# Performance work log

Hardware: AMD Instinct MI355X
Metric: run time of the kernel (lower is better)

Reference implementation:

```python
import jax, jax.numpy as jnp
import numpy as np

B_SZ, N_NODES, C_IN, C_OUT, M_EDGES, DEG = 32, 4096, 64, 64, 64, 256
E_INC = M_EDGES * DEG  # 16384 incidences
NEG_SLOPE = 0.2
MARGIN = 4.2


def setup_inputs() -> dict:
    key = jax.random.key(0)
    k1, k2, k3, k4 = jax.random.split(key, 4)
    x = jax.random.normal(k1, (B_SZ, N_NODES, C_IN), jnp.float32)
    # glorot-ish params
    weight = jax.random.normal(k2, (C_IN, C_OUT), jnp.float32) * (1.0 / np.sqrt(C_IN))
    att = jax.random.normal(k3, (1, 1, 2 * C_OUT), jnp.float32) * 0.1
    node_ids = jax.random.randint(k4, (E_INC,), 0, N_NODES, dtype=jnp.int32)
    edge_ids = jnp.repeat(jnp.arange(M_EDGES, dtype=jnp.int32), DEG)  # sorted, all edges present
    hyperedge_index = jnp.stack([node_ids, edge_ids], axis=0)
    return {"x": x, "weight": weight, "att": att,
            "hyperedge_index": hyperedge_index,
            "num_edges": M_EDGES, "num_nodes": N_NODES}


def _segment_softmax(scores, seg, num_segments):
    m = jax.ops.segment_max(scores, seg, num_segments=num_segments)
    e = jnp.exp(scores - m[seg])
    s = jax.ops.segment_sum(e, seg, num_segments=num_segments)
    return e / s[seg]


def reference(x, weight, att, hyperedge_index, num_edges, num_nodes):
    node_ids = hyperedge_index[0]
    edge_ids = hyperedge_index[1]
    M = num_edges
    N = num_nodes

    xw = jnp.einsum('bnc,cd->bnd', x, weight)       # [B,N,C]
    x1 = jnp.swapaxes(xw, 0, 1)                     # [N,B,C]

    x_i = x1[node_ids]                              # [E,B,C] gather per incidence
    edge_sums = jax.ops.segment_sum(x_i, edge_ids, num_segments=M,
                                    indices_are_sorted=True)  # [M,B,C]
    x_j = edge_sums[edge_ids]                       # [E,B,C]

    # pairwise hyperedge contrastive loss (vectorized double loop over edges)
    inner = jnp.einsum('kbc,mbc->kmb', edge_sums, edge_sums)          # [M,M,B]
    nrm = jnp.linalg.norm(edge_sums, axis=-1)                         # [M,B]
    cos = inner / (nrm[:, None, :] * nrm[None, :, :])                 # [M,M,B]
    diff = edge_sums[:, None] - edge_sums[None, :]                    # [M,M,B,C]
    dist = jnp.linalg.norm(diff, axis=-1)                             # [M,M,B]
    loss_item = cos * dist + (1.0 - cos) * jnp.clip(MARGIN - dist, 0.0)
    loss_hyper = jnp.sum(jnp.abs(jnp.mean(loss_item, axis=2))) / (M + 1) ** 2

    # GAT-style attention over incidences, softmax grouped by node
    cat = jnp.concatenate([x_i, x_j], axis=-1)                        # [E,B,2C]
    scores = jnp.sum(cat * att[0], axis=-1)                           # [E,B] (heads=1)
    scores = jax.nn.leaky_relu(scores, negative_slope=NEG_SLOPE)
    alpha = _segment_softmax(scores, node_ids, N)                     # [E,B]
    # dropout omitted (eval mode)

    ones = jnp.ones((node_ids.shape[0],), xw.dtype)
    D = jax.ops.segment_sum(ones, node_ids, num_segments=N)           # node degree
    deg_e = jax.ops.segment_sum(ones, edge_ids, num_segments=M, indices_are_sorted=True)
    B_norm = jnp.where(deg_e > 0, 1.0 / deg_e, 0.0)                   # 1/edge degree, inf->0

    # stage 1: nodes -> hyperedges (source_to_target)
    msg1 = B_norm[edge_ids][:, None, None] * (alpha[..., None] * x_i) # [E,B,C]
    out_e = jax.ops.segment_sum(msg1, edge_ids, num_segments=M, indices_are_sorted=True)
    # stage 2: hyperedges -> nodes (target_to_source)
    msg2 = D[node_ids][:, None, None] * (alpha[..., None] * out_e[edge_ids])
    out_n = jax.ops.segment_sum(msg2, node_ids, num_segments=N)       # [N,B,C]

    out = jnp.swapaxes(out_n, 0, 1)                                   # [B,N,C]
    constrain_total = jnp.abs(jnp.mean(x_i - x_j)) + loss_hyper
    return out, constrain_total
```

## Files before the change

kernel.cpp:

```cpp
#include <hip/hip_runtime.h>
#include <math.h>

#define B_SZ 32
#define N_NODES 4096
#define C_DIM 64
#define M_EDGES 64
#define DEG 256
#define E_INC 16384
#define NEG_SLOPE 0.2f
#define MARGIN 4.2f

__device__ __forceinline__ float wsum64(float v) {
#pragma unroll
  for (int off = 32; off > 0; off >>= 1) v += __shfl_xor(v, off, 64);
  return v;
}

__device__ __forceinline__ float4 redq16_32(float4 a) {
#pragma unroll
  for (int off = 16; off < 64; off <<= 1) {
    a.x += __shfl_xor(a.x, off, 64);
    a.y += __shfl_xor(a.y, off, 64);
    a.z += __shfl_xor(a.z, off, 64);
    a.w += __shfl_xor(a.w, off, 64);
  }
  return a;
}

union SmemBig {
  struct {
    float wl[4096];
    float sx[4][64];
    float sxc[64];
  } e;
  struct {
    int cnt[N_NODES];
  } c;
  struct {
    float part[4][64];
    float wattl[64];
  } s;
};

__global__ __launch_bounds__(256) void k_p1(
    const float* __restrict__ x, const float* __restrict__ w,
    const float* __restrict__ att, const int* __restrict__ node_ids,
    float* __restrict__ s1_t, float* __restrict__ es_t,
    float* __restrict__ s2, float* __restrict__ nrm2,
    float* __restrict__ essum, int* __restrict__ cntv) {
  __shared__ SmemBig sm;
  const int bid = blockIdx.x;
  const int t = threadIdx.x;
  if (bid < 2048) {
    const int b = 4 * (bid & 7) + ((bid >> 3) & 3);
    const int m = bid >> 5;
    const int lane = t & 63, wv = t >> 6;
    const int qc = lane & 15, rsub = lane >> 4;
    float4* wl4 = (float4*)sm.e.wl;
    const float4* w4 = (const float4*)w;
#pragma unroll
    for (int i = 0; i < 4; ++i) wl4[t + 256 * i] = w4[t + 256 * i];
    const float4* xb4 = (const float4*)(x + (size_t)b * (N_NODES * C_DIM));
    const int rbase = m * DEG + wv * 64 + rsub;
    float4 acc = {0.f, 0.f, 0.f, 0.f};
#pragma unroll
    for (int i = 0; i < 16; ++i) {
      const int node = node_ids[rbase + i * 4];
      const float4 xv = xb4[node * 16 + qc];
      acc.x += xv.x;
      acc.y += xv.y;
      acc.z += xv.z;
      acc.w += xv.w;
    }
    acc = redq16_32(acc);
    if (rsub == 0) ((float4*)sm.e.sx[wv])[qc] = acc;
    __syncthreads();
    if (t < 64) {
      sm.e.sxc[t] =
          sm.e.sx[0][t] + sm.e.sx[1][t] + sm.e.sx[2][t] + sm.e.sx[3][t];
      float es = 0.f;
#pragma unroll 8
      for (int j = 0; j < 64; ++j)
        es = fmaf(sm.e.sxc[j], sm.e.wl[j * 64 + t], es);
      es_t[(m * 64 + t) * 32 + b] = es;
      const float sr = wsum64(es * att[64 + t]);
      const float nr = wsum64(es * es);
      const float er = wsum64(es);
      if (t == 0) {
        s2[m * 32 + b] = sr;
        nrm2[m * 32 + b] = nr;
        essum[m * 32 + b] = er;
      }
    }
  } else if (bid < 2112) {
    const int m = bid - 2048;
#pragma unroll
    for (int i = 0; i < 16; ++i) sm.c.cnt[t + 256 * i] = 0;
    __syncthreads();
    atomicAdd(&sm.c.cnt[node_ids[m * DEG + t]], 1);
    __syncthreads();
#pragma unroll
    for (int i = 0; i < 16; ++i)
      cntv[m * N_NODES + t + 256 * i] = sm.c.cnt[t + 256 * i];
  } else {
    const int sb = bid - 2112;
    const int kk = t & 63, q = t >> 6;
    float p = 0.f;
#pragma unroll
    for (int c = 0; c < 16; ++c)
      p = fmaf(w[kk * 64 + q * 16 + c], att[q * 16 + c], p);
    sm.s.part[q][kk] = p;
    __syncthreads();
    if (t < 64)
      sm.s.wattl[t] =
          sm.s.part[0][t] + sm.s.part[1][t] + sm.s.part[2][t] + sm.s.part[3][t];
    __syncthreads();
    const int lane = t & 63, wv = t >> 6;
    const int kq = lane & 15, rsub = lane >> 4;
    const float4 wq = ((const float4*)sm.s.wattl)[kq];
    const int r0 = sb * 256 + wv * 64;
#pragma unroll 4
    for (int it = 0; it < 16; ++it) {
      const int row = r0 + it * 4 + rsub;
      const float4 xv = ((const float4*)x)[row * 16 + kq];
      float vv = xv.x * wq.x + xv.y * wq.y + xv.z * wq.z + xv.w * wq.w;
      vv += __shfl_xor(vv, 1, 64);
      vv += __shfl_xor(vv, 2, 64);
      vv += __shfl_xor(vv, 4, 64);
      vv += __shfl_xor(vv, 8, 64);
      if (kq == 0) {
        const int n = row & (N_NODES - 1);
        const int b = row >> 12;
        s1_t[n * 32 + b] = vv;
      }
    }
  }
}

__global__ __launch_bounds__(256) void k_p2(
    const float* __restrict__ es_t, const float* __restrict__ nrm2,
    const int* __restrict__ cntv, const float* __restrict__ s1_t,
    const float* __restrict__ s2, float* __restrict__ lossbuf,
    float2* __restrict__ pnb) {
  const int bid = blockIdx.x;
  if (bid < 1024) {
    const int wv = threadIdx.x >> 6;
    const int p = bid * 4 + wv;
    const int k = p >> 6, m = p & 63;
    const int lane = threadIdx.x & 63;
    const int b = lane & 31, ch = lane >> 5;
    float inner = 0.f;
#pragma unroll 8
    for (int cc = 0; cc < 32; ++cc) {
      const int c = cc + 32 * ch;
      inner = fmaf(es_t[(k * 64 + c) * 32 + b], es_t[(m * 64 + c) * 32 + b],
                   inner);
    }
    inner += __shfl_xor(inner, 32, 64);
    const float nk2 = nrm2[k * 32 + b];
    const float nm2 = nrm2[m * 32 + b];
    const float d2 = fmaxf(nk2 + nm2 - 2.f * inner, 0.f);
    const float dist = sqrtf(d2);
    const float cosv = inner / sqrtf(nk2 * nm2);
    float li = cosv * dist + (1.f - cosv) * fmaxf(MARGIN - dist, 0.f);
#pragma unroll
    for (int off = 16; off > 0; off >>= 1) li += __shfl_xor(li, off, 64);
    if (lane == 0) lossbuf[p] = fabsf(li * (1.f / 32.f));
  } else {
    const int idx = (bid - 1024) * 256 + threadIdx.x;
    const int n = idx >> 5, b = idx & 31;
    const float s1v = s1_t[n * 32 + b];
    float mx = -1e30f, S = 0.f;
#pragma unroll 4
    for (int m = 0; m < 64; ++m) {
      const int cm = cntv[m * N_NODES + n];
      if (cm > 0) {
        float sc = s1v + s2[m * 32 + b];
        sc = sc > 0.f ? sc : NEG_SLOPE * sc;
        const float nm = fmaxf(mx, sc);
        S = S * __expf(mx - nm) + (float)cm * __expf(sc - nm);
        mx = nm;
      }
    }
    float2 pv;
    pv.x = mx;
    pv.y = (S > 0.f) ? 1.f / S : 0.f;
    pnb[n * 32 + b] = pv;
  }
}

__global__ __launch_bounds__(256) void k_p3(
    const float* __restrict__ x, const int* __restrict__ node_ids,
    const float* __restrict__ w, const float* __restrict__ s1_t,
    const float* __restrict__ s2, const float2* __restrict__ pnb,
    const float* __restrict__ essum, const float* __restrict__ lossbuf,
    float* __restrict__ out_e_t, float* __restrict__ outs) {
  __shared__ SmemBig sm;
  const int bid = blockIdx.x;
  const int t = threadIdx.x;
  if (bid < 2048) {
    const int b = 4 * (bid & 7) + ((bid >> 3) & 3);
    const int m = bid >> 5;
    const int lane = t & 63, wv = t >> 6;
    const int qc = lane & 15, rsub = lane >> 4;
    float4* wl4 = (float4*)sm.e.wl;
    const float4* w4 = (const float4*)w;
#pragma unroll
    for (int i = 0; i < 4; ++i) wl4[t + 256 * i] = w4[t + 256 * i];
    const float4* xb4 = (const float4*)(x + (size_t)b * (N_NODES * C_DIM));
    const float s2mb = s2[m * 32 + b];
    const int rbase = m * DEG + wv * 64 + rsub;
    float4 acc = {0.f, 0.f, 0.f, 0.f};
#pragma unroll
    for (int i = 0; i < 16; ++i) {
      const int node = node_ids[rbase + i * 4];
      const float s1v = s1_t[node * 32 + b];
      const float2 pv = pnb[node * 32 + b];
      float sc = s1v + s2mb;
      sc = sc > 0.f ? sc : NEG_SLOPE * sc;
      const float a = __expf(sc - pv.x) * pv.y;
      const float4 xv = xb4[node * 16 + qc];
      acc.x = fmaf(a, xv.x, acc.x);
      acc.y = fmaf(a, xv.y, acc.y);
      acc.z = fmaf(a, xv.z, acc.z);
      acc.w = fmaf(a, xv.w, acc.w);
    }
    acc = redq16_32(acc);
    if (rsub == 0) ((float4*)sm.e.sx[wv])[qc] = acc;
    __syncthreads();
    if (t < 64) {
      sm.e.sxc[t] =
          sm.e.sx[0][t] + sm.e.sx[1][t] + sm.e.sx[2][t] + sm.e.sx[3][t];
      float oc = 0.f;
#pragma unroll 8
      for (int j = 0; j < 64; ++j)
        oc = fmaf(sm.e.sxc[j], sm.e.wl[j * 64 + t], oc);
      out_e_t[(m * 64 + t) * 32 + b] = oc * (1.0f / 256.0f);
    }
  } else {
    __shared__ float smf[256];
    float s = 0.f;
    for (int i = t; i < M_EDGES * B_SZ; i += 256) s += essum[i];
    smf[t] = s;
    __syncthreads();
    for (int o = 128; o > 0; o >>= 1) {
      if (t < o) smf[t] += smf[t + o];
      __syncthreads();
    }
    const float S = smf[0];
    __syncthreads();
    float l = 0.f;
    for (int i = t; i < M_EDGES * M_EDGES; i += 256) l += lossbuf[i];
    smf[t] = l;
    __syncthreads();
    for (int o = 128; o > 0; o >>= 1) {
      if (t < o) smf[t] += smf[t + o];
      __syncthreads();
    }
    if (t == 0) {
      const float mean = S * (-255.0f) / 33554432.0f;
      outs[0] = fabsf(mean) + smf[0] * (1.0f / 4225.0f);
    }
  }
}

__global__ __launch_bounds__(256) void k_p4(
    const int* __restrict__ cntv, const float* __restrict__ s1_t,
    const float* __restrict__ s2, const float2* __restrict__ pnb,
    const float* __restrict__ out_e_t, float* __restrict__ out) {
  __shared__ int listm[64];
  __shared__ int cl[64];
  __shared__ float al[64][32];
  __shared__ float DnS;
  __shared__ int llenS;
  const int n = blockIdx.x;
  const int t = threadIdx.x;
  if (t < 64) {
    const int cv = cntv[t * N_NODES + n];
    cl[t] = cv;
    const unsigned long long mask = __ballot(cv > 0);
    const int pos = __popcll(mask & ((1ull << t) - 1ull));
    if (cv > 0) listm[pos] = t;
    const float d = wsum64((float)cv);
    if (t == 0) {
      llenS = __popcll(mask);
      DnS = d;
    }
  }
  __syncthreads();
  const int llen = llenS;
  const int c = t & 63, bq = t >> 6;
  const size_t nb = (size_t)n * 64 + c;
  const size_t st = (size_t)N_NODES * 64;
  if (llen == 0) {
#pragma unroll
    for (int j = 0; j < 8; ++j) out[(bq * 8 + j) * st + nb] = 0.f;
    return;
  }
  {
    const int b = t & 31, lq = t >> 5;
    const float s1v = s1_t[n * 32 + b];
    const float2 pv = pnb[n * 32 + b];
    for (int base = 0; base < llen; base += 8) {
      const int li = base + lq;
      if (li < llen) {
        const int m = listm[li];
        float sc = s1v + s2[m * 32 + b];
        sc = sc > 0.f ? sc : NEG_SLOPE * sc;
        al[li][b] = (float)cl[m] * __expf(sc - pv.x) * pv.y;
      }
    }
  }
  __syncthreads();
  float4 a0 = {0.f, 0.f, 0.f, 0.f}, a1 = {0.f, 0.f, 0.f, 0.f};
  for (int li = 0; li < llen; ++li) {
    const int m = listm[li];
    const float4 v0 = *(const float4*)&out_e_t[(m * 64 + c) * 32 + bq * 8];
    const float4 v1 = *(const float4*)&out_e_t[(m * 64 + c) * 32 + bq * 8 + 4];
    const float* alr = al[li];
    a0.x = fmaf(alr[bq * 8 + 0], v0.x, a0.x);
    a0.y = fmaf(alr[bq * 8 + 1], v0.y, a0.y);
    a0.z = fmaf(alr[bq * 8 + 2], v0.z, a0.z);
    a0.w = fmaf(alr[bq * 8 + 3], v0.w, a0.w);
    a1.x = fmaf(alr[bq * 8 + 4], v1.x, a1.x);
    a1.y = fmaf(alr[bq * 8 + 5], v1.y, a1.y);
    a1.z = fmaf(alr[bq * 8 + 6], v1.z, a1.z);
    a1.w = fmaf(alr[bq * 8 + 7], v1.w, a1.w);
  }
  const float Dn = DnS;
  out[(bq * 8 + 0) * st + nb] = Dn * a0.x;
  out[(bq * 8 + 1) * st + nb] = Dn * a0.y;
  out[(bq * 8 + 2) * st + nb] = Dn * a0.z;
  out[(bq * 8 + 3) * st + nb] = Dn * a0.w;
  out[(bq * 8 + 4) * st + nb] = Dn * a1.x;
  out[(bq * 8 + 5) * st + nb] = Dn * a1.y;
  out[(bq * 8 + 6) * st + nb] = Dn * a1.z;
  out[(bq * 8 + 7) * st + nb] = Dn * a1.w;
}

extern "C" void kernel_launch(void* const* d_in, const int* in_sizes, int n_in,
                              void* d_out, int out_size, void* d_ws,
                              size_t ws_size, hipStream_t stream) {
  (void)in_sizes; (void)n_in; (void)out_size; (void)ws_size;
  const float* x = (const float*)d_in[0];
  const float* weight = (const float*)d_in[1];
  const float* att = (const float*)d_in[2];
  const int* node_ids = (const int*)d_in[3];
  float* out = (float*)d_out;

  char* wsb = (char*)d_ws;
  float* es_t = (float*)(wsb);
  float* out_e_t = (float*)(wsb + (512 << 10));
  float* s1_t = (float*)(wsb + (1024 << 10));
  int* cntv = (int*)(wsb + (1536 << 10));
  float2* pnb = (float2*)(wsb + (2560 << 10));
  float* s2 = (float*)(wsb + (3584 << 10));
  float* nrm2 = (float*)(wsb + (3592 << 10));
  float* essum = (float*)(wsb + (3600 << 10));
  float* lossbuf = (float*)(wsb + (3608 << 10));

  k_p1<<<2624, 256, 0, stream>>>(x, weight, att, node_ids, s1_t, es_t, s2,
                                 nrm2, essum, cntv);
  k_p2<<<1536, 256, 0, stream>>>(es_t, nrm2, cntv, s1_t, s2, lossbuf, pnb);
  k_p3<<<2049, 256, 0, stream>>>(x, node_ids, weight, s1_t, s2, pnb, essum,
                                 lossbuf, out_e_t,
                                 out + (size_t)B_SZ * N_NODES * C_DIM);
  k_p4<<<4096, 256, 0, stream>>>(cntv, s1_t, s2, pnb, out_e_t, out);
}
```

Baseline: 91.44 us.

## Fuse attention score into gather, exploit loss symmetry, precompute node edge lists

New measurement: 102.7 us. +12.3%, slower.

```diff
diff --git a/kernel.cpp b/kernel.cpp
--- a/kernel.cpp
+++ b/kernel.cpp
@@ -27,19 +27,9 @@
   return a;
 }
 
-union SmemBig {
-  struct {
-    float wl[4096];
-    float sx[4][64];
-    float sxc[64];
-  } e;
-  struct {
-    int cnt[N_NODES];
-  } c;
-  struct {
-    float part[4][64];
-    float wattl[64];
-  } s;
+union U16K {
+  float wl[4096];
+  int cnt[4096];
 };
 
 __global__ __launch_bounds__(256) void k_p1(
@@ -48,7 +38,11 @@
     float* __restrict__ s1_t, float* __restrict__ es_t,
     float* __restrict__ s2, float* __restrict__ nrm2,
     float* __restrict__ essum, int* __restrict__ cntv) {
-  __shared__ SmemBig sm;
+  __shared__ U16K u;
+  __shared__ float part[4][64];
+  __shared__ float wattl[64];
+  __shared__ float sx[4][64];
+  __shared__ float sxc[64];
   const int bid = blockIdx.x;
   const int t = threadIdx.x;
   if (bid < 2048) {
@@ -56,10 +50,23 @@
     const int m = bid >> 5;
     const int lane = t & 63, wv = t >> 6;
     const int qc = lane & 15, rsub = lane >> 4;
-    float4* wl4 = (float4*)sm.e.wl;
+    float4* wl4 = (float4*)u.wl;
     const float4* w4 = (const float4*)w;
 #pragma unroll
     for (int i = 0; i < 4; ++i) wl4[t + 256 * i] = w4[t + 256 * i];
+    {
+      const int kk = t & 63, q = t >> 6;
+      float p = 0.f;
+#pragma unroll
+      for (int c = 0; c < 16; ++c)
+        p = fmaf(w[kk * 64 + q * 16 + c], att[q * 16 + c], p);
+      part[q][kk] = p;
+    }
+    __syncthreads();
+    if (t < 64)
+      wattl[t] = part[0][t] + part[1][t] + part[2][t] + part[3][t];
+    __syncthreads();
+    const float4 wq = ((const float4*)wattl)[qc];
     const float4* xb4 = (const float4*)(x + (size_t)b * (N_NODES * C_DIM));
     const int rbase = m * DEG + wv * 64 + rsub;
     float4 acc = {0.f, 0.f, 0.f, 0.f};
@@ -71,17 +78,21 @@
       acc.y += xv.y;
       acc.z += xv.z;
       acc.w += xv.w;
+      float sv = xv.x * wq.x + xv.y * wq.y + xv.z * wq.z + xv.w * wq.w;
+      sv += __shfl_xor(sv, 1, 64);
+      sv += __shfl_xor(sv, 2, 64);
+      sv += __shfl_xor(sv, 4, 64);
+      sv += __shfl_xor(sv, 8, 64);
+      if (qc == 0) s1_t[node * 32 + b] = sv;
     }
     acc = redq16_32(acc);
-    if (rsub == 0) ((float4*)sm.e.sx[wv])[qc] = acc;
+    if (rsub == 0) ((float4*)sx[wv])[qc] = acc;
     __syncthreads();
     if (t < 64) {
-      sm.e.sxc[t] =
-          sm.e.sx[0][t] + sm.e.sx[1][t] + sm.e.sx[2][t] + sm.e.sx[3][t];
+      sxc[t] = sx[0][t] + sx[1][t] + sx[2][t] + sx[3][t];
       float es = 0.f;
 #pragma unroll 8
-      for (int j = 0; j < 64; ++j)
-        es = fmaf(sm.e.sxc[j], sm.e.wl[j * 64 + t], es);
+      for (int j = 0; j < 64; ++j) es = fmaf(sxc[j], u.wl[j * 64 + t], es);
       es_t[(m * 64 + t) * 32 + b] = es;
       const float sr = wsum64(es * att[64 + t]);
       const float nr = wsum64(es * es);
@@ -92,61 +103,35 @@
         essum[m * 32 + b] = er;
       }
     }
-  } else if (bid < 2112) {
+  } else {
     const int m = bid - 2048;
 #pragma unroll
-    for (int i = 0; i < 16; ++i) sm.c.cnt[t + 256 * i] = 0;
-    __syncthreads();
-    atomicAdd(&sm.c.cnt[node_ids[m * DEG + t]], 1);
+    for (int i = 0; i < 16; ++i) u.cnt[t + 256 * i] = 0;
+    __syncthreads();
+    atomicAdd(&u.cnt[node_ids[m * DEG + t]], 1);
     __syncthreads();
 #pragma unroll
     for (int i = 0; i < 16; ++i)
-      cntv[m * N_NODES + t + 256 * i] = sm.c.cnt[t + 256 * i];
-  } else {
-    const int sb = bid - 2112;
-    const int kk = t & 63, q = t >> 6;
-    float p = 0.f;
-#pragma unroll
-    for (int c = 0; c < 16; ++c)
-      p = fmaf(w[kk * 64 + q * 16 + c], att[q * 16 + c], p);
-    sm.s.part[q][kk] = p;
-    __syncthreads();
-    if (t < 64)
-      sm.s.wattl[t] =
-          sm.s.part[0][t] + sm.s.part[1][t] + sm.s.part[2][t] + sm.s.part[3][t];
-    __syncthreads();
-    const int lane = t & 63, wv = t >> 6;
-    const int kq = lane & 15, rsub = lane >> 4;
-    const float4 wq = ((const float4*)sm.s.wattl)[kq];
-    const int r0 = sb * 256 + wv * 64;
-#pragma unroll 4
-    for (int it = 0; it < 16; ++it) {
-      const int row = r0 + it * 4 + rsub;
-      const float4 xv = ((const float4*)x)[row * 16 + kq];
-      float vv = xv.x * wq.x + xv.y * wq.y + xv.z * wq.z + xv.w * wq.w;
-      vv += __shfl_xor(vv, 1, 64);
-      vv += __shfl_xor(vv, 2, 64);
-      vv += __shfl_xor(vv, 4, 64);
-      vv += __shfl_xor(vv, 8, 64);
-      if (kq == 0) {
-        const int n = row & (N_NODES - 1);
-        const int b = row >> 12;
-        s1_t[n * 32 + b] = vv;
-      }
-    }
+      cntv[m * N_NODES + t + 256 * i] = u.cnt[t + 256 * i];
   }
 }
 
 __global__ __launch_bounds__(256) void k_p2(
     const float* __restrict__ es_t, const float* __restrict__ nrm2,
     const int* __restrict__ cntv, const float* __restrict__ s1_t,
-    const float* __restrict__ s2, float* __restrict__ lossbuf,
-    float2* __restrict__ pnb) {
+    const float* __restrict__ s2, float* __restrict__ lossbuf2,
+    float2* __restrict__ pnb, int* __restrict__ pdat,
+    int* __restrict__ plen) {
   const int bid = blockIdx.x;
-  if (bid < 1024) {
+  if (bid < 504) {
     const int wv = threadIdx.x >> 6;
     const int p = bid * 4 + wv;
-    const int k = p >> 6, m = p & 63;
+    int k = 0, off = 0;
+    while (off + (63 - k) <= p) {
+      off += 63 - k;
+      ++k;
+    }
+    const int m = k + 1 + (p - off);
     const int lane = threadIdx.x & 63;
     const int b = lane & 31, ch = lane >> 5;
     float inner = 0.f;
@@ -164,24 +149,33 @@
     const float cosv = inner / sqrtf(nk2 * nm2);
     float li = cosv * dist + (1.f - cosv) * fmaxf(MARGIN - dist, 0.f);
 #pragma unroll
-    for (int off = 16; off > 0; off >>= 1) li += __shfl_xor(li, off, 64);
-    if (lane == 0) lossbuf[p] = fabsf(li * (1.f / 32.f));
+    for (int o = 16; o > 0; o >>= 1) li += __shfl_xor(li, o, 64);
+    if (lane == 0) lossbuf2[p] = 2.f * fabsf(li * (1.f / 32.f));
   } else {
-    const int idx = (bid - 1024) * 256 + threadIdx.x;
+    const int idx = (bid - 504) * 256 + threadIdx.x;
     const int n = idx >> 5, b = idx & 31;
     const float s1v = s1_t[n * 32 + b];
+    const bool leader = (b == 0);
     float mx = -1e30f, S = 0.f;
+    int j = 0, Dsum = 0;
 #pragma unroll 4
     for (int m = 0; m < 64; ++m) {
       const int cm = cntv[m * N_NODES + n];
-      if (cm > 0) {
-        float sc = s1v + s2[m * 32 + b];
-        sc = sc > 0.f ? sc : NEG_SLOPE * sc;
-        const float nm = fmaxf(mx, sc);
-        S = S * __expf(mx - nm) + (float)cm * __expf(sc - nm);
-        mx = nm;
+      float sc = s1v + s2[m * 32 + b];
+      sc = sc > 0.f ? sc : NEG_SLOPE * sc;
+      const float scv = (cm > 0) ? sc : -1e30f;
+      const float nm = fmaxf(mx, scv);
+      S = S * __expf(mx - nm) + (float)cm * __expf(scv - nm);
+      mx = nm;
+      if (leader) {
+        if (cm > 0) {
+          pdat[n * 64 + j] = m | (cm << 8);
+          ++j;
+        }
+        Dsum += cm;
       }
     }
+    if (leader) plen[n] = j | (Dsum << 7);
     float2 pv;
     pv.x = mx;
     pv.y = (S > 0.f) ? 1.f / S : 0.f;
@@ -193,9 +187,11 @@
     const float* __restrict__ x, const int* __restrict__ node_ids,
     const float* __restrict__ w, const float* __restrict__ s1_t,
     const float* __restrict__ s2, const float2* __restrict__ pnb,
-    const float* __restrict__ essum, const float* __restrict__ lossbuf,
+    const float* __restrict__ essum, const float* __restrict__ lossbuf2,
     float* __restrict__ out_e_t, float* __restrict__ outs) {
-  __shared__ SmemBig sm;
+  __shared__ U16K u;
+  __shared__ float sx[4][64];
+  __shared__ float sxc[64];
   const int bid = blockIdx.x;
   const int t = threadIdx.x;
   if (bid < 2048) {
@@ -203,7 +199,7 @@
     const int m = bid >> 5;
     const int lane = t & 63, wv = t >> 6;
     const int qc = lane & 15, rsub = lane >> 4;
-    float4* wl4 = (float4*)sm.e.wl;
+    float4* wl4 = (float4*)u.wl;
     const float4* w4 = (const float4*)w;
 #pragma unroll
     for (int i = 0; i < 4; ++i) wl4[t + 256 * i] = w4[t + 256 * i];
@@ -226,15 +222,13 @@
       acc.w = fmaf(a, xv.w, acc.w);
     }
     acc = redq16_32(acc);
-    if (rsub == 0) ((float4*)sm.e.sx[wv])[qc] = acc;
+    if (rsub == 0) ((float4*)sx[wv])[qc] = acc;
     __syncthreads();
     if (t < 64) {
-      sm.e.sxc[t] =
-          sm.e.sx[0][t] + sm.e.sx[1][t] + sm.e.sx[2][t] + sm.e.sx[3][t];
+      sxc[t] = sx[0][t] + sx[1][t] + sx[2][t] + sx[3][t];
       float oc = 0.f;
 #pragma unroll 8
-      for (int j = 0; j < 64; ++j)
-        oc = fmaf(sm.e.sxc[j], sm.e.wl[j * 64 + t], oc);
+      for (int j = 0; j < 64; ++j) oc = fmaf(sxc[j], u.wl[j * 64 + t], oc);
       out_e_t[(m * 64 + t) * 32 + b] = oc * (1.0f / 256.0f);
     }
   } else {
@@ -250,7 +244,7 @@
     const float S = smf[0];
     __syncthreads();
     float l = 0.f;
-    for (int i = t; i < M_EDGES * M_EDGES; i += 256) l += lossbuf[i];
+    for (int i = t; i < 2016; i += 256) l += lossbuf2[i];
     smf[t] = l;
     __syncthreads();
     for (int o = 128; o > 0; o >>= 1) {
@@ -265,56 +259,50 @@
 }
 
 __global__ __launch_bounds__(256) void k_p4(
-    const int* __restrict__ cntv, const float* __restrict__ s1_t,
-    const float* __restrict__ s2, const float2* __restrict__ pnb,
-    const float* __restrict__ out_e_t, float* __restrict__ out) {
-  __shared__ int listm[64];
-  __shared__ int cl[64];
+    const int* __restrict__ plen, const int* __restrict__ pdat,
+    const float* __restrict__ s1_t, const float* __restrict__ s2,
+    const float2* __restrict__ pnb, const float* __restrict__ out_e_t,
+    float* __restrict__ out) {
+  __shared__ int lme[64];
+  __shared__ float lcnt[64];
   __shared__ float al[64][32];
-  __shared__ float DnS;
-  __shared__ int llenS;
   const int n = blockIdx.x;
   const int t = threadIdx.x;
-  if (t < 64) {
-    const int cv = cntv[t * N_NODES + n];
-    cl[t] = cv;
-    const unsigned long long mask = __ballot(cv > 0);
-    const int pos = __popcll(mask & ((1ull << t) - 1ull));
-    if (cv > 0) listm[pos] = t;
-    const float d = wsum64((float)cv);
-    if (t == 0) {
-      llenS = __popcll(mask);
-      DnS = d;
-    }
-  }
-  __syncthreads();
-  const int llen = llenS;
+  const int pl = plen[n];
+  const int len = pl & 127;
+  const float Dn = (float)(pl >> 7);
   const int c = t & 63, bq = t >> 6;
   const size_t nb = (size_t)n * 64 + c;
   const size_t st = (size_t)N_NODES * 64;
-  if (llen == 0) {
+  if (len == 0) {
 #pragma unroll
     for (int j = 0; j < 8; ++j) out[(bq * 8 + j) * st + nb] = 0.f;
     return;
   }
+  if (t < len) {
+    const int pe = pdat[n * 64 + t];
+    lme[t] = pe & 63;
+    lcnt[t] = (float)(pe >> 8);
+  }
+  __syncthreads();
   {
     const int b = t & 31, lq = t >> 5;
     const float s1v = s1_t[n * 32 + b];
     const float2 pv = pnb[n * 32 + b];
-    for (int base = 0; base < llen; base += 8) {
+    for (int base = 0; base < len; base += 8) {
       const int li = base + lq;
-      if (li < llen) {
-        const int m = listm[li];
+      if (li < len) {
+        const int m = lme[li];
         float sc = s1v + s2[m * 32 + b];
         sc = sc > 0.f ? sc : NEG_SLOPE * sc;
-        al[li][b] = (float)cl[m] * __expf(sc - pv.x) * pv.y;
+        al[li][b] = lcnt[li] * __expf(sc - pv.x) * pv.y;
       }
     }
   }
   __syncthreads();
   float4 a0 = {0.f, 0.f, 0.f, 0.f}, a1 = {0.f, 0.f, 0.f, 0.f};
-  for (int li = 0; li < llen; ++li) {
-    const int m = listm[li];
+  for (int li = 0; li < len; ++li) {
+    const int m = lme[li];
     const float4 v0 = *(const float4*)&out_e_t[(m * 64 + c) * 32 + bq * 8];
     const float4 v1 = *(const float4*)&out_e_t[(m * 64 + c) * 32 + bq * 8 + 4];
     const float* alr = al[li];
@@ -327,7 +315,6 @@
     a1.z = fmaf(alr[bq * 8 + 6], v1.z, a1.z);
     a1.w = fmaf(alr[bq * 8 + 7], v1.w, a1.w);
   }
-  const float Dn = DnS;
   out[(bq * 8 + 0) * st + nb] = Dn * a0.x;
   out[(bq * 8 + 1) * st + nb] = Dn * a0.y;
   out[(bq * 8 + 2) * st + nb] = Dn * a0.z;
@@ -354,16 +341,19 @@
   float* s1_t = (float*)(wsb + (1024 << 10));
   int* cntv = (int*)(wsb + (1536 << 10));
   float2* pnb = (float2*)(wsb + (2560 << 10));
-  float* s2 = (float*)(wsb + (3584 << 10));
-  float* nrm2 = (float*)(wsb + (3592 << 10));
-  float* essum = (float*)(wsb + (3600 << 10));
-  float* lossbuf = (float*)(wsb + (3608 << 10));
-
-  k_p1<<<2624, 256, 0, stream>>>(x, weight, att, node_ids, s1_t, es_t, s2,
+  int* pdat = (int*)(wsb + (3584 << 10));
+  float* s2 = (float*)(wsb + (4608 << 10));
+  float* nrm2 = (float*)(wsb + (4616 << 10));
+  float* essum = (float*)(wsb + (4624 << 10));
+  float* lossbuf2 = (float*)(wsb + (4632 << 10));
+  int* plen = (int*)(wsb + (4640 << 10));
+
+  k_p1<<<2112, 256, 0, stream>>>(x, weight, att, node_ids, s1_t, es_t, s2,
                                  nrm2, essum, cntv);
-  k_p2<<<1536, 256, 0, stream>>>(es_t, nrm2, cntv, s1_t, s2, lossbuf, pnb);
+  k_p2<<<1016, 256, 0, stream>>>(es_t, nrm2, cntv, s1_t, s2, lossbuf2, pnb,
+                                 pdat, plen);
   k_p3<<<2049, 256, 0, stream>>>(x, node_ids, weight, s1_t, s2, pnb, essum,
-                                 lossbuf, out_e_t,
+                                 lossbuf2, out_e_t,
                                  out + (size_t)B_SZ * N_NODES * C_DIM);
-  k_p4<<<4096, 256, 0, stream>>>(cntv, s1_t, s2, pnb, out_e_t, out);
-}
+  k_p4<<<4096, 256, 0, stream>>>(plen, pdat, s1_t, s2, pnb, out_e_t, out);
+}
```
